# Optimization experiments

Measured on AMD Instinct MI355X. Metric: run time of the kernel, lower is better.

The kernel has to match this reference:

```python
import jax, jax.numpy as jnp
import numpy as np

EPS = 1e-5
NUM_GN_GROUPS = 32


def setup_inputs() -> dict:
    key = jax.random.key(0)
    k1, k2, k3 = jax.random.split(key, 3)
    B, C, N, G = 2, 256, 4096, 8
    c = C // G
    return {
        "points": jax.random.normal(k1, (B, C, N), dtype=jnp.float32),
        "conv_w": jax.random.normal(k2, (G, c, c), dtype=jnp.float32) / np.sqrt(c),
        "conv_b": jax.random.normal(k3, (C,), dtype=jnp.float32) * 0.02,
        "gn_w": jnp.ones((C,), dtype=jnp.float32),
        "gn_b": jnp.zeros((C,), dtype=jnp.float32),
    }


def reference(points, conv_w, conv_b, gn_w, gn_b):
    B, C, N = points.shape
    G = conv_w.shape[0]
    c = C // G  # channels per attention group
    identity = points

    # grouped 1x1 conv: per-group [c,c] matmul + bias
    x = points.reshape(B, G, c, N)
    x = jnp.einsum('gij,bgjn->bgin', conv_w, x) + conv_b.reshape(1, G, c, 1)

    # attention[b,g,n,m] = sum_i x[b,g,i,n] * x[b,g,i,m] / sqrt(c)
    scale = 1.0 / np.sqrt(c).astype(np.float32)
    attn = jnp.einsum('bgin,bgim->bgnm', x, x) * scale
    # softmax over dim=2 (the query/row N axis -- non-standard)
    attn = jax.nn.softmax(attn, axis=2)

    # ELU-gated second matmul: [B,G,c,N] @ [B,G,N,N] -> [B,G,c,N]
    x = jnp.einsum('bgcn,bgnm->bgcm', jax.nn.elu(x), attn)

    # channel shuffle: [B,G,c,N] -> [B,c,G,N] -> [B,C,N]
    x = x.transpose(0, 2, 1, 3).reshape(B, C, N)
    x = x + identity

    # GroupNorm(32 groups) over (channels-in-group, N)
    xg = x.reshape(B, NUM_GN_GROUPS, C // NUM_GN_GROUPS, N)
    mean = xg.mean(axis=(2, 3), keepdims=True)
    var = xg.var(axis=(2, 3), keepdims=True)
    xg = (xg - mean) * jax.lax.rsqrt(var + EPS)
    x = xg.reshape(B, C, N)
    return x * gn_w.reshape(1, C, 1) + gn_b.reshape(1, C, 1)
```

## Files before the change

kernel.cpp:

```cpp
#include <hip/hip_runtime.h>

typedef __attribute__((ext_vector_type(8))) short bf16x8;
typedef __attribute__((ext_vector_type(4))) short bf16x4;
typedef __attribute__((ext_vector_type(4))) float f32x4;

#if __has_builtin(__builtin_amdgcn_exp2f)
#define EXP2(x) __builtin_amdgcn_exp2f(x)
#else
#define EXP2(x) exp2f(x)
#endif

__device__ __forceinline__ unsigned short f2bf(float f) {
    union { float f; unsigned int u; } v; v.f = f;
    unsigned int r = v.u + 0x7fffu + ((v.u >> 16) & 1u);
    return (unsigned short)(r >> 16);
}

__device__ __forceinline__ float asf(unsigned int u) {
    union { unsigned int u; float f; } v; v.u = u; return v.f;
}

#define QK_PRESCALE 0.50500983f

__global__ __launch_bounds__(256) void conv_kernel(
    const float* __restrict__ points, const float* __restrict__ conv_w,
    const float* __restrict__ conv_b,
    unsigned short* __restrict__ xqT, unsigned short* __restrict__ xv)
{
    __shared__ float w[1024];
    const int h  = blockIdx.x >> 6;
    const int nc = blockIdx.x & 63;
    const int g  = h & 7;
    const int tid = threadIdx.x;
    const float* wg = conv_w + g * 1024;
    for (int k = tid; k < 1024; k += 256) w[k] = wg[k];
    __syncthreads();
    const int n  = nc * 64 + (tid & 63);
    const int ig = tid >> 6;
    const float* p = points + (size_t)h * 32 * 4096 + n;
    float pv[32];
#pragma unroll
    for (int j = 0; j < 32; ++j) pv[j] = p[(size_t)j * 4096];
    float out[8];
#pragma unroll
    for (int ii = 0; ii < 8; ++ii) {
        const int i = ig * 8 + ii;
        float acc = conv_b[g * 32 + i];
        const float4* w4 = (const float4*)(w + i * 32);
#pragma unroll
        for (int j4 = 0; j4 < 8; ++j4) {
            float4 ww = w4[j4];
            acc += ww.x * pv[j4 * 4]     + ww.y * pv[j4 * 4 + 1]
                 + ww.z * pv[j4 * 4 + 2] + ww.w * pv[j4 * 4 + 3];
        }
        out[ii] = acc;
    }
    unsigned short tq[8];
#pragma unroll
    for (int ii = 0; ii < 8; ++ii) tq[ii] = f2bf(out[ii] * QK_PRESCALE);
    *(bf16x8*)(xqT + ((size_t)h * 4096 + n) * 32 + ig * 8) = *(bf16x8*)tq;
#pragma unroll
    for (int ii = 0; ii < 8; ++ii) {
        float x = out[ii];
        float e = x > 0.f ? x : (__expf(x) - 1.f);
        xv[((size_t)h * 32 + ig * 8 + ii) * 4096 + n] = f2bf(e);
    }
}

#define VSTR 136
#define PSTR 72

#if __has_builtin(__builtin_amdgcn_cvt_pk_bf16_f32)
typedef __attribute__((ext_vector_type(2))) __bf16 bf16x2v;
__device__ __forceinline__ bf16x4 exp_pack(f32x4 sc, float& lsum) {
    float e0 = EXP2(sc[0]), e1 = EXP2(sc[1]);
    float e2 = EXP2(sc[2]), e3 = EXP2(sc[3]);
    lsum += (e0 + e1) + (e2 + e3);
    union { bf16x2v v[2]; bf16x4 s; } u;
    u.v[0] = __builtin_amdgcn_cvt_pk_bf16_f32(e0, e1);
    u.v[1] = __builtin_amdgcn_cvt_pk_bf16_f32(e2, e3);
    return u.s;
}
#else
__device__ __forceinline__ bf16x4 exp_pack(f32x4 sc, float& lsum) {
    union { float f; unsigned int u; } e0, e1, e2, e3;
    e0.f = EXP2(sc[0]); e1.f = EXP2(sc[1]); e2.f = EXP2(sc[2]); e3.f = EXP2(sc[3]);
    unsigned int t0 = e0.u & 0xffff0000u, t1 = e1.u & 0xffff0000u;
    unsigned int t2 = e2.u & 0xffff0000u, t3 = e3.u & 0xffff0000u;
    lsum += (asf(t0) + asf(t1)) + (asf(t2) + asf(t3));
    union { unsigned int d[2]; bf16x4 v; } pk;
    pk.d[0] = (t0 >> 16) | t1;
    pk.d[1] = (t2 >> 16) | t3;
    return pk.v;
}
#endif

#define CHUNK(C0, KU, KP)                                                      \
    {                                                                          \
        __syncthreads();                                                       \
        *(bf16x8*)(Vt + vi * VSTR + vn)      = va;                             \
        *(bf16x8*)(Vt + vi * VSTR + vn + 64) = vb;                             \
        __syncthreads();                                                       \
        const int pfb = ((C0) + 128) & 2047;                                   \
        va = *(const bf16x8*)(vbaseh + (size_t)vi * 4096 + pfb + vn);          \
        vb = *(const bf16x8*)(vbaseh + (size_t)vi * 4096 + pfb + vn + 64);     \
        _Pragma("unroll")                                                      \
        for (int s8 = 0; s8 < 8; ++s8)                                         \
            KP[s8] = *(const bf16x8*)(kfph + (size_t)(pfb + s8 * 16) * 32);    \
        _Pragma("unroll")                                                      \
        for (int sub = 0; sub < 2; ++sub) {                                    \
            _Pragma("unroll")                                                  \
            for (int s = 0; s < 4; ++s) {                                      \
                f32x4 sc = __builtin_amdgcn_mfma_f32_16x16x32_bf16(            \
                    KU[sub * 4 + s], qfrag, (f32x4){0.f, 0.f, 0.f, 0.f},       \
                    0, 0, 0);                                                  \
                bf16x4 pk = exp_pack(sc, lsum);                                \
                *(bf16x4*)(pw + l15 * PSTR + s * 16 + quad * 4) = pk;          \
            }                                                                  \
            _Pragma("unroll")                                                  \
            for (int ng = 0; ng < 2; ++ng) {                                   \
                bf16x8 pfrag = *(const bf16x8*)(pw + l15 * PSTR + ng * 32 +    \
                                                quad * 8);                     \
                const int col = sub * 64 + ng * 32 + quad * 8;                 \
                bf16x8 v0 = *(const bf16x8*)(Vt + l15 * VSTR + col);           \
                bf16x8 v1 = *(const bf16x8*)(Vt + (16 + l15) * VSTR + col);    \
                acc0 = __builtin_amdgcn_mfma_f32_16x16x32_bf16(v0, pfrag,      \
                                                               acc0, 0, 0, 0); \
                acc1 = __builtin_amdgcn_mfma_f32_16x16x32_bf16(v1, pfrag,      \
                                                               acc1, 0, 0, 0); \
            }                                                                  \
        }                                                                      \
    }

__global__ __launch_bounds__(256, 4) void attn_kernel(
    const unsigned short* __restrict__ xqT,
    const unsigned short* __restrict__ xv,
    float* __restrict__ opart, float* __restrict__ lpart)
{
    __shared__ unsigned short Vt[32 * VSTR];
    __shared__ unsigned short Pl[4][16 * PSTR];

    const int bid = blockIdx.x;
    const int x  = bid & 7;
    const int r  = bid >> 3;
    const int h  = x * 2 + (r & 1);
    const int rr = r >> 1;
    const int qt = rr & 63;
    const int kh = rr >> 6;
    const int tid = threadIdx.x;
    const int wv = tid >> 6, lane = tid & 63;
    const int quad = lane >> 4, l15 = lane & 15;

    const int m = qt * 64 + wv * 16 + l15;

    const unsigned short* kbase = xqT + (size_t)h * 4096 * 32;
    const unsigned short* vbaseh = xv + (size_t)h * 32 * 4096 + kh * 2048;

    const bf16x8 qfrag = *(const bf16x8*)(kbase + (size_t)m * 32 + quad * 8);

    f32x4 acc0 = {0.f, 0.f, 0.f, 0.f};
    f32x4 acc1 = {0.f, 0.f, 0.f, 0.f};
    float lsum = 0.f;

    const int vi = tid >> 3, vn = (tid & 7) * 8;
    unsigned short* pw = &Pl[wv][0];

    const unsigned short* kfph =
        kbase + ((size_t)kh * 2048 + l15) * 32 + quad * 8;

    bf16x8 va = *(const bf16x8*)(vbaseh + (size_t)vi * 4096 + vn);
    bf16x8 vb = *(const bf16x8*)(vbaseh + (size_t)vi * 4096 + vn + 64);
    bf16x8 kA[8], kB[8];
#pragma unroll
    for (int s8 = 0; s8 < 8; ++s8)
        kA[s8] = *(const bf16x8*)(kfph + (size_t)(s8 * 16) * 32);

    for (int n0 = 0; n0 < 2048; n0 += 256) {
        CHUNK(n0,       kA, kB);
        CHUNK(n0 + 128, kB, kA);
    }

    lsum += __shfl_xor(lsum, 16, 64);
    lsum += __shfl_xor(lsum, 32, 64);

    const int ml = wv * 16 + l15;
    const size_t hq2 = ((size_t)h * 64 + qt) * 2 + kh;
    float* ob = opart + hq2 * 2048;
#pragma unroll
    for (int half = 0; half < 2; ++half) {
        f32x4 a = half ? acc1 : acc0;
#pragma unroll
        for (int rr2 = 0; rr2 < 4; ++rr2) {
            const int i = half * 16 + quad * 4 + rr2;
            ob[i * 64 + ml] = a[rr2];
        }
    }
    if (quad == 0) lpart[hq2 * 64 + ml] = lsum;
}

__global__ __launch_bounds__(256) void combine_kernel(
    const float* __restrict__ opart, const float* __restrict__ lpart,
    const float* __restrict__ points, float* __restrict__ z,
    float* __restrict__ pstats)
{
    const int bid2 = blockIdx.x;
    const int h = bid2 >> 6, qt = bid2 & 63;
    const int b = h >> 3, g = h & 7;
    const int tid = threadIdx.x;
    const int w = tid >> 6, lane = tid & 63;
    const int mg = qt * 64 + lane;

    const float la = lpart[(size_t)(bid2 * 2) * 64 + lane];
    const float lb = lpart[(size_t)(bid2 * 2 + 1) * 64 + lane];
    const float inv = 1.f / (la + lb);

    const float* oa = opart + (size_t)(bid2 * 2) * 2048;
    const float* obp = opart + (size_t)(bid2 * 2 + 1) * 2048;
    const float* pb = points + (size_t)b * 256 * 4096;
    float* zb = z + (size_t)b * 256 * 4096;
    float* sb = pstats + (size_t)bid2 * 64;

#pragma unroll
    for (int ii = 0; ii < 8; ++ii) {
        const int i = w * 8 + ii;
        const size_t off = (size_t)(i * 8 + g) * 4096 + mg;
        float v = (oa[i * 64 + lane] + obp[i * 64 + lane]) * inv + pb[off];
        zb[off] = v;
        float s = v, ss = v * v;
        s += __shfl_xor(s, 1, 64);   ss += __shfl_xor(ss, 1, 64);
        s += __shfl_xor(s, 2, 64);   ss += __shfl_xor(ss, 2, 64);
        s += __shfl_xor(s, 4, 64);   ss += __shfl_xor(ss, 4, 64);
        s += __shfl_xor(s, 8, 64);   ss += __shfl_xor(ss, 8, 64);
        s += __shfl_xor(s, 16, 64);  ss += __shfl_xor(ss, 16, 64);
        s += __shfl_xor(s, 32, 64);  ss += __shfl_xor(ss, 32, 64);
        if (lane == 0) { sb[i * 2] = s; sb[i * 2 + 1] = ss; }
    }
}

__global__ __launch_bounds__(256) void gn_combine(const float* __restrict__ pstats,
                                                  float* __restrict__ stats)
{
    const int b = blockIdx.x >> 5;
    const int i = blockIdx.x & 31;
    const int tid = threadIdx.x;
    float s = 0.f, ss = 0.f;
    for (int k = tid; k < 512; k += 256) {
        const float* p = pstats + (size_t)(b * 512 + k) * 64 + i * 2;
        s += p[0]; ss += p[1];
    }
#pragma unroll
    for (int off = 32; off > 0; off >>= 1) {
        s  += __shfl_down(s, off, 64);
        ss += __shfl_down(ss, off, 64);
    }
    __shared__ float red[8];
    const int w = tid >> 6;
    if ((tid & 63) == 0) { red[w * 2] = s; red[w * 2 + 1] = ss; }
    __syncthreads();
    if (tid == 0) {
        s  = red[0] + red[2] + red[4] + red[6];
        ss = red[1] + red[3] + red[5] + red[7];
        float mean = s * (1.f / 32768.f);
        float var  = ss * (1.f / 32768.f) - mean * mean;
        stats[blockIdx.x * 2]     = mean;
        stats[blockIdx.x * 2 + 1] = rsqrtf(var + 1e-5f);
    }
}

__global__ __launch_bounds__(256) void gn_apply(float* __restrict__ z,
                                                const float* __restrict__ stats,
                                                const float* __restrict__ gw,
                                                const float* __restrict__ gb)
{
    const int idx = blockIdx.x * 256 + threadIdx.x;
    float4* p = (float4*)z;
    float4 v = p[idx];
    const int chg = idx >> 10;
    const int blk = chg >> 3;
    const int ch  = chg & 255;
    const float mean = stats[blk * 2], rstd = stats[blk * 2 + 1];
    const float w  = gw[ch] * rstd;
    const float bb = gb[ch] - mean * w;
    v.x = v.x * w + bb; v.y = v.y * w + bb;
    v.z = v.z * w + bb; v.w = v.w * w + bb;
    p[idx] = v;
}

extern "C" void kernel_launch(void* const* d_in, const int* in_sizes, int n_in,
                              void* d_out, int out_size, void* d_ws, size_t ws_size,
                              hipStream_t stream)
{
    const float* points = (const float*)d_in[0];
    const float* conv_w = (const float*)d_in[1];
    const float* conv_b = (const float*)d_in[2];
    const float* gn_w   = (const float*)d_in[3];
    const float* gn_b   = (const float*)d_in[4];
    float* out = (float*)d_out;
    char* ws = (char*)d_ws;
    const size_t MB = 1024 * 1024;
    unsigned short* xqT = (unsigned short*)ws;
    unsigned short* xv  = (unsigned short*)(ws + 4 * MB);
    float* opart  = (float*)(ws + 8 * MB);
    float* lpart  = (float*)(ws + 24 * MB);
    float* pstats = (float*)(ws + 25 * MB);
    float* stats  = (float*)(ws + 26 * MB);

    conv_kernel<<<1024, 256, 0, stream>>>(points, conv_w, conv_b, xqT, xv);
    attn_kernel<<<2048, 256, 0, stream>>>(xqT, xv, opart, lpart);
    combine_kernel<<<1024, 256, 0, stream>>>(opart, lpart, points, out, pstats);
    gn_combine<<<64, 256, 0, stream>>>(pstats, stats);
    gn_apply<<<2048, 256, 0, stream>>>(out, stats, gn_w, gn_b);
}
```

Before: 160.3 us.

## Double query tile per wave and stage keys through shared memory

Each wave now processes two 16-row query fragments (128 queries per block instead of 64), so every key/value fragment loaded feeds twice as many MFMAs. Keys are now staged cooperatively into LDS with a padded stride instead of each wave loading its own register-resident key fragments from global memory. The grid is halved, and the combine and GN-stat kernels are reindexed to the new partial-output layout. This raises register and LDS use per block, which may lower occupancy, and halves the number of blocks available to fill the CUs.

```diff
diff --git a/kernel.cpp b/kernel.cpp
--- a/kernel.cpp
+++ b/kernel.cpp
@@ -67,6 +67,7 @@
     }
 }
 
+#define KSTR 40
 #define VSTR 136
 #define PSTR 72
 
@@ -95,107 +96,113 @@
 }
 #endif
 
-#define CHUNK(C0, KU, KP)                                                      \
-    {                                                                          \
-        __syncthreads();                                                       \
-        *(bf16x8*)(Vt + vi * VSTR + vn)      = va;                             \
-        *(bf16x8*)(Vt + vi * VSTR + vn + 64) = vb;                             \
-        __syncthreads();                                                       \
-        const int pfb = ((C0) + 128) & 2047;                                   \
-        va = *(const bf16x8*)(vbaseh + (size_t)vi * 4096 + pfb + vn);          \
-        vb = *(const bf16x8*)(vbaseh + (size_t)vi * 4096 + pfb + vn + 64);     \
-        _Pragma("unroll")                                                      \
-        for (int s8 = 0; s8 < 8; ++s8)                                         \
-            KP[s8] = *(const bf16x8*)(kfph + (size_t)(pfb + s8 * 16) * 32);    \
-        _Pragma("unroll")                                                      \
-        for (int sub = 0; sub < 2; ++sub) {                                    \
-            _Pragma("unroll")                                                  \
-            for (int s = 0; s < 4; ++s) {                                      \
-                f32x4 sc = __builtin_amdgcn_mfma_f32_16x16x32_bf16(            \
-                    KU[sub * 4 + s], qfrag, (f32x4){0.f, 0.f, 0.f, 0.f},       \
-                    0, 0, 0);                                                  \
-                bf16x4 pk = exp_pack(sc, lsum);                                \
-                *(bf16x4*)(pw + l15 * PSTR + s * 16 + quad * 4) = pk;          \
-            }                                                                  \
-            _Pragma("unroll")                                                  \
-            for (int ng = 0; ng < 2; ++ng) {                                   \
-                bf16x8 pfrag = *(const bf16x8*)(pw + l15 * PSTR + ng * 32 +    \
-                                                quad * 8);                     \
-                const int col = sub * 64 + ng * 32 + quad * 8;                 \
-                bf16x8 v0 = *(const bf16x8*)(Vt + l15 * VSTR + col);           \
-                bf16x8 v1 = *(const bf16x8*)(Vt + (16 + l15) * VSTR + col);    \
-                acc0 = __builtin_amdgcn_mfma_f32_16x16x32_bf16(v0, pfrag,      \
-                                                               acc0, 0, 0, 0); \
-                acc1 = __builtin_amdgcn_mfma_f32_16x16x32_bf16(v1, pfrag,      \
-                                                               acc1, 0, 0, 0); \
-            }                                                                  \
-        }                                                                      \
-    }
-
 __global__ __launch_bounds__(256, 4) void attn_kernel(
     const unsigned short* __restrict__ xqT,
     const unsigned short* __restrict__ xv,
     float* __restrict__ opart, float* __restrict__ lpart)
 {
+    __shared__ unsigned short Kt[128 * KSTR];
     __shared__ unsigned short Vt[32 * VSTR];
-    __shared__ unsigned short Pl[4][16 * PSTR];
+    __shared__ unsigned short Pl[4][32 * PSTR];
 
     const int bid = blockIdx.x;
     const int x  = bid & 7;
     const int r  = bid >> 3;
     const int h  = x * 2 + (r & 1);
     const int rr = r >> 1;
-    const int qt = rr & 63;
-    const int kh = rr >> 6;
+    const int qt = rr & 31;
+    const int kh = rr >> 5;
     const int tid = threadIdx.x;
     const int wv = tid >> 6, lane = tid & 63;
     const int quad = lane >> 4, l15 = lane & 15;
 
-    const int m = qt * 64 + wv * 16 + l15;
-
-    const unsigned short* kbase = xqT + (size_t)h * 4096 * 32;
+    const int mA = qt * 128 + wv * 32 + l15;
+    const int mB = mA + 16;
+
+    const unsigned short* kbase  = xqT + (size_t)h * 4096 * 32;
+    const unsigned short* khalf  = kbase + (size_t)kh * 2048 * 32;
     const unsigned short* vbaseh = xv + (size_t)h * 32 * 4096 + kh * 2048;
 
-    const bf16x8 qfrag = *(const bf16x8*)(kbase + (size_t)m * 32 + quad * 8);
-
-    f32x4 acc0 = {0.f, 0.f, 0.f, 0.f};
-    f32x4 acc1 = {0.f, 0.f, 0.f, 0.f};
-    float lsum = 0.f;
-
+    const bf16x8 qfragA = *(const bf16x8*)(kbase + (size_t)mA * 32 + quad * 8);
+    const bf16x8 qfragB = *(const bf16x8*)(kbase + (size_t)mB * 32 + quad * 8);
+
+    f32x4 accA0 = {0,0,0,0}, accA1 = {0,0,0,0};
+    f32x4 accB0 = {0,0,0,0}, accB1 = {0,0,0,0};
+    float lsumA = 0.f, lsumB = 0.f;
+
+    const int kr = tid >> 2, kc = (tid & 3) * 8;
     const int vi = tid >> 3, vn = (tid & 7) * 8;
     unsigned short* pw = &Pl[wv][0];
 
-    const unsigned short* kfph =
-        kbase + ((size_t)kh * 2048 + l15) * 32 + quad * 8;
-
+    bf16x8 ka = *(const bf16x8*)(khalf + (size_t)kr * 32 + kc);
+    bf16x8 kb = *(const bf16x8*)(khalf + (size_t)(64 + kr) * 32 + kc);
     bf16x8 va = *(const bf16x8*)(vbaseh + (size_t)vi * 4096 + vn);
     bf16x8 vb = *(const bf16x8*)(vbaseh + (size_t)vi * 4096 + vn + 64);
-    bf16x8 kA[8], kB[8];
-#pragma unroll
-    for (int s8 = 0; s8 < 8; ++s8)
-        kA[s8] = *(const bf16x8*)(kfph + (size_t)(s8 * 16) * 32);
-
-    for (int n0 = 0; n0 < 2048; n0 += 256) {
-        CHUNK(n0,       kA, kB);
-        CHUNK(n0 + 128, kB, kA);
-    }
-
-    lsum += __shfl_xor(lsum, 16, 64);
-    lsum += __shfl_xor(lsum, 32, 64);
-
-    const int ml = wv * 16 + l15;
-    const size_t hq2 = ((size_t)h * 64 + qt) * 2 + kh;
-    float* ob = opart + hq2 * 2048;
+
+    for (int n0 = 0; n0 < 2048; n0 += 128) {
+        __syncthreads();
+        *(bf16x8*)(Kt + kr * KSTR + kc)        = ka;
+        *(bf16x8*)(Kt + (kr + 64) * KSTR + kc) = kb;
+        *(bf16x8*)(Vt + vi * VSTR + vn)        = va;
+        *(bf16x8*)(Vt + vi * VSTR + vn + 64)   = vb;
+        __syncthreads();
+        const int pfb = (n0 + 128) & 2047;
+        ka = *(const bf16x8*)(khalf + (size_t)(pfb + kr) * 32 + kc);
+        kb = *(const bf16x8*)(khalf + (size_t)(pfb + 64 + kr) * 32 + kc);
+        va = *(const bf16x8*)(vbaseh + (size_t)vi * 4096 + pfb + vn);
+        vb = *(const bf16x8*)(vbaseh + (size_t)vi * 4096 + pfb + vn + 64);
+
+#pragma unroll
+        for (int sub = 0; sub < 2; ++sub) {
+#pragma unroll
+            for (int s = 0; s < 4; ++s) {
+                bf16x8 kf = *(const bf16x8*)(
+                    Kt + (sub * 64 + s * 16 + l15) * KSTR + quad * 8);
+                f32x4 scA = __builtin_amdgcn_mfma_f32_16x16x32_bf16(
+                    kf, qfragA, (f32x4){0,0,0,0}, 0, 0, 0);
+                f32x4 scB = __builtin_amdgcn_mfma_f32_16x16x32_bf16(
+                    kf, qfragB, (f32x4){0,0,0,0}, 0, 0, 0);
+                bf16x4 pkA = exp_pack(scA, lsumA);
+                bf16x4 pkB = exp_pack(scB, lsumB);
+                *(bf16x4*)(pw + l15 * PSTR + s * 16 + quad * 4) = pkA;
+                *(bf16x4*)(pw + (16 + l15) * PSTR + s * 16 + quad * 4) = pkB;
+            }
+#pragma unroll
+            for (int ng = 0; ng < 2; ++ng) {
+                bf16x8 pfA = *(const bf16x8*)(pw + l15 * PSTR + ng * 32 + quad * 8);
+                bf16x8 pfB = *(const bf16x8*)(pw + (16 + l15) * PSTR + ng * 32 + quad * 8);
+                const int col = sub * 64 + ng * 32 + quad * 8;
+                bf16x8 v0 = *(const bf16x8*)(Vt + l15 * VSTR + col);
+                bf16x8 v1 = *(const bf16x8*)(Vt + (16 + l15) * VSTR + col);
+                accA0 = __builtin_amdgcn_mfma_f32_16x16x32_bf16(v0, pfA, accA0, 0, 0, 0);
+                accA1 = __builtin_amdgcn_mfma_f32_16x16x32_bf16(v1, pfA, accA1, 0, 0, 0);
+                accB0 = __builtin_amdgcn_mfma_f32_16x16x32_bf16(v0, pfB, accB0, 0, 0, 0);
+                accB1 = __builtin_amdgcn_mfma_f32_16x16x32_bf16(v1, pfB, accB1, 0, 0, 0);
+            }
+        }
+    }
+
+    lsumA += __shfl_xor(lsumA, 16, 64);  lsumA += __shfl_xor(lsumA, 32, 64);
+    lsumB += __shfl_xor(lsumB, 16, 64);  lsumB += __shfl_xor(lsumB, 32, 64);
+
+    const size_t slot = (((size_t)h * 32 + qt) * 2 + kh);
+    float* ob = opart + slot * 4096;
+    const int mlA = wv * 32 + l15, mlB = mlA + 16;
 #pragma unroll
     for (int half = 0; half < 2; ++half) {
-        f32x4 a = half ? acc1 : acc0;
-#pragma unroll
-        for (int rr2 = 0; rr2 < 4; ++rr2) {
-            const int i = half * 16 + quad * 4 + rr2;
-            ob[i * 64 + ml] = a[rr2];
+        f32x4 aA = half ? accA1 : accA0;
+        f32x4 aB = half ? accB1 : accB0;
+#pragma unroll
+        for (int r2 = 0; r2 < 4; ++r2) {
+            const int i = half * 16 + quad * 4 + r2;
+            ob[i * 128 + mlA] = aA[r2];
+            ob[i * 128 + mlB] = aB[r2];
         }
     }
-    if (quad == 0) lpart[hq2 * 64 + ml] = lsum;
+    if (quad == 0) {
+        lpart[slot * 128 + mlA] = lsumA;
+        lpart[slot * 128 + mlB] = lsumB;
+    }
 }
 
 __global__ __launch_bounds__(256) void combine_kernel(
@@ -204,29 +211,33 @@
     float* __restrict__ pstats)
 {
     const int bid2 = blockIdx.x;
-    const int h = bid2 >> 6, qt = bid2 & 63;
+    const int h = bid2 >> 5, qt = bid2 & 31;
     const int b = h >> 3, g = h & 7;
     const int tid = threadIdx.x;
     const int w = tid >> 6, lane = tid & 63;
-    const int mg = qt * 64 + lane;
-
-    const float la = lpart[(size_t)(bid2 * 2) * 64 + lane];
-    const float lb = lpart[(size_t)(bid2 * 2 + 1) * 64 + lane];
-    const float inv = 1.f / (la + lb);
-
-    const float* oa = opart + (size_t)(bid2 * 2) * 2048;
-    const float* obp = opart + (size_t)(bid2 * 2 + 1) * 2048;
+
+    const size_t sl0 = (size_t)bid2 * 2;
+    const float inv0 = 1.f / (lpart[sl0 * 128 + lane] +
+                              lpart[(sl0 + 1) * 128 + lane]);
+    const float inv1 = 1.f / (lpart[sl0 * 128 + 64 + lane] +
+                              lpart[(sl0 + 1) * 128 + 64 + lane]);
+
+    const float* oa  = opart + sl0 * 4096;
+    const float* obp = opart + (sl0 + 1) * 4096;
     const float* pb = points + (size_t)b * 256 * 4096;
     float* zb = z + (size_t)b * 256 * 4096;
     float* sb = pstats + (size_t)bid2 * 64;
+    const int mg0 = qt * 128 + lane, mg1 = mg0 + 64;
 
 #pragma unroll
     for (int ii = 0; ii < 8; ++ii) {
         const int i = w * 8 + ii;
-        const size_t off = (size_t)(i * 8 + g) * 4096 + mg;
-        float v = (oa[i * 64 + lane] + obp[i * 64 + lane]) * inv + pb[off];
-        zb[off] = v;
-        float s = v, ss = v * v;
+        const size_t off = (size_t)(i * 8 + g) * 4096;
+        float v0 = (oa[i * 128 + lane]      + obp[i * 128 + lane])      * inv0 + pb[off + mg0];
+        float v1 = (oa[i * 128 + 64 + lane] + obp[i * 128 + 64 + lane]) * inv1 + pb[off + mg1];
+        zb[off + mg0] = v0;
+        zb[off + mg1] = v1;
+        float s = v0 + v1, ss = v0 * v0 + v1 * v1;
         s += __shfl_xor(s, 1, 64);   ss += __shfl_xor(ss, 1, 64);
         s += __shfl_xor(s, 2, 64);   ss += __shfl_xor(ss, 2, 64);
         s += __shfl_xor(s, 4, 64);   ss += __shfl_xor(ss, 4, 64);
@@ -243,11 +254,8 @@
     const int b = blockIdx.x >> 5;
     const int i = blockIdx.x & 31;
     const int tid = threadIdx.x;
-    float s = 0.f, ss = 0.f;
-    for (int k = tid; k < 512; k += 256) {
-        const float* p = pstats + (size_t)(b * 512 + k) * 64 + i * 2;
-        s += p[0]; ss += p[1];
-    }
+    const float* p = pstats + (size_t)(b * 256 + tid) * 64 + i * 2;
+    float s = p[0], ss = p[1];
 #pragma unroll
     for (int off = 32; off > 0; off >>= 1) {
         s  += __shfl_down(s, off, 64);
@@ -306,8 +314,8 @@
     float* stats  = (float*)(ws + 26 * MB);
 
     conv_kernel<<<1024, 256, 0, stream>>>(points, conv_w, conv_b, xqT, xv);
-    attn_kernel<<<2048, 256, 0, stream>>>(xqT, xv, opart, lpart);
-    combine_kernel<<<1024, 256, 0, stream>>>(opart, lpart, points, out, pstats);
+    attn_kernel<<<1024, 256, 0, stream>>>(xqT, xv, opart, lpart);
+    combine_kernel<<<512, 256, 0, stream>>>(opart, lpart, points, out, pstats);
     gn_combine<<<64, 256, 0, stream>>>(pstats, stats);
     gn_apply<<<2048, 256, 0, stream>>>(out, stats, gn_w, gn_b);
 }
```

New measurement: 174.8 us. 1.09x slower.
